# Optimization experiments

Measured on AMD Instinct MI355X. Metric: run time of the kernel, lower is better.

## Reference

```python
import jax, jax.numpy as jnp
import numpy as np

SEQ_LEN, BATCH, INPUT, HID, LAYERS, TARGET_LEN = 120, 2048, 6, 64, 4, 120


def _cell(x_t, h, c, Wih, Whh, b):
    # torch LSTM gate order: input, forget, cell(g), output
    gates = x_t @ Wih.T + h @ Whh.T + b  # [B, 4H]
    i, f, g, o = jnp.split(gates, 4, axis=-1)
    c_new = jax.nn.sigmoid(f) * c + jax.nn.sigmoid(i) * jnp.tanh(g)
    h_new = jax.nn.sigmoid(o) * jnp.tanh(c_new)
    return h_new, c_new


def _stack_step(h, c, x_t, Wih0, Wih, Whh, b):
    # one time step through all stacked layers; h, c: [L, B, H]
    hs, cs = [], []
    inp = x_t
    L = Whh.shape[0]
    for l in range(L):
        W = Wih0 if l == 0 else Wih[l - 1]
        hn, cn = _cell(inp, h[l], c[l], W, Whh[l], b[l])
        hs.append(hn)
        cs.append(cn)
        inp = hn
    return jnp.stack(hs), jnp.stack(cs), inp


def setup_inputs() -> dict:
    key = jax.random.key(0)
    ks = jax.random.split(key, 11)
    s = 1.0 / np.sqrt(HID)  # torch LSTM uniform init scale
    u = lambda k, shp: jax.random.uniform(k, shp, jnp.float32, -s, s)
    return {
        "x": jax.random.normal(ks[0], (SEQ_LEN, BATCH, INPUT), jnp.float32),
        "enc_Wih0": u(ks[1], (4 * HID, INPUT)),
        "enc_Wih": u(ks[2], (LAYERS - 1, 4 * HID, HID)),
        "enc_Whh": u(ks[3], (LAYERS, 4 * HID, HID)),
        "enc_b": u(ks[4], (LAYERS, 4 * HID)),
        "dec_Wih0": u(ks[5], (4 * HID, INPUT)),
        "dec_Wih": u(ks[6], (LAYERS - 1, 4 * HID, HID)),
        "dec_Whh": u(ks[7], (LAYERS, 4 * HID, HID)),
        "dec_b": u(ks[8], (LAYERS, 4 * HID)),
        "lin_W": u(ks[9], (INPUT, HID)),
        "lin_b": u(ks[10], (INPUT,)),
        "target_len": TARGET_LEN,
    }


def reference(x, enc_Wih0, enc_Wih, enc_Whh, enc_b,
              dec_Wih0, dec_Wih, dec_Whh, dec_b, lin_W, lin_b, target_len):
    L, B, H = enc_Whh.shape[0], x.shape[1], enc_Whh.shape[-1]
    h0 = jnp.zeros((L, B, H), x.dtype)

    # ---- encoder: stacked LSTM over the input sequence (zero init state) ----
    def enc_step(carry, x_t):
        h, c = carry
        h, c, _ = _stack_step(h, c, x_t, enc_Wih0, enc_Wih, enc_Whh, enc_b)
        return (h, c), None

    (h, c), _ = jax.lax.scan(enc_step, (h0, h0), x)

    # ---- decoder: recursive one-step decode for target_len steps ----
    def dec_step(carry, _):
        h, c, inp = carry
        h, c, top = _stack_step(h, c, inp, dec_Wih0, dec_Wih, dec_Whh, dec_b)
        out = top @ lin_W.T + lin_b  # [B, INPUT]
        return (h, c, out), out

    last_in = x[-1]  # decoder seeded with last observed frame
    _, outputs = jax.lax.scan(dec_step, (h, c, last_in), None, length=target_len)
    return outputs  # [target_len, B, INPUT]
```

## Files before the change

### kernel.cpp

```cpp
#include <hip/hip_runtime.h>


#define S_LEN 120
#define BATCH 2048
#define NIN   6
#define H     64
#define NL    4
#define TLEN  120

#define HPAD 72

#define FRAGS_HALF 60
#define PACK_H8    (2 * FRAGS_HALF * 4 * 64)
#define PROJ_H8    (2 * 64)
#define NPACK      ((PACK_H8 + PROJ_H8) * 8)
#define EPACK_EL   (256 * 64 * 8)
#define NTOT       (NPACK + EPACK_EL)

#define PERM(kk) ((((kk) & 3) << 4) | ((kk) >> 2))
#define PI(c)    ((((c) & 15) << 2) | ((c) >> 4))

typedef _Float16 h8    __attribute__((ext_vector_type(8)));
typedef _Float16 h4    __attribute__((ext_vector_type(4)));
typedef float    f32x4 __attribute__((ext_vector_type(4)));

__device__ __forceinline__ void bar_lgkm() {
  asm volatile("s_waitcnt lgkmcnt(0)\n\ts_barrier" ::: "memory");
}

__global__ void prep_weights(const float* __restrict__ eWih0,
                             const float* __restrict__ eWih,
                             const float* __restrict__ eWhh,
                             const float* __restrict__ dWih0,
                             const float* __restrict__ dWih,
                             const float* __restrict__ dWhh,
                             const float* __restrict__ linW,
                             _Float16* __restrict__ wq) {
  int idx = blockIdx.x * blockDim.x + threadIdx.x;
  if (idx >= NTOT) return;

  if (idx >= NPACK) {
    int p    = idx - NPACK;
    int j    = p & 7;
    int lane = (p >> 3) & 63;
    int fe   = p >> 9;
    int kt   = fe & 3, nt = (fe >> 2) & 15, l = fe >> 6;
    int g    = nt * 16 + (lane & 15);
    int koff = ((lane >> 4) << 3) + j;
    float v = 0.0f;
    if (l == 0) {
      if (kt == 0)      v = (koff < NIN) ? eWih0[g * NIN + koff] : 0.0f;
      else if (kt == 1) v = 0.0f;
      else { int kk = (kt - 2) * 32 + koff; v = eWhh[g * H + PERM(kk)]; }
    } else {
      if (kt < 2) { int kk = kt * 32 + koff;
                    v = eWih[((l - 1) * 256 + g) * H + PERM(kk)]; }
      else        { int kk = (kt - 2) * 32 + koff;
                    v = eWhh[(l * 256 + g) * H + PERM(kk)]; }
    }
    wq[idx] = (_Float16)v;
    return;
  }

  if (idx >= PACK_H8 * 8) {
    int p    = idx - PACK_H8 * 8;
    int j    = p & 7;
    int lane = (p >> 3) & 63;
    int fr   = p >> 9;
    int m    = lane & 15;
    int k    = fr * 32 + ((lane >> 4) << 3) + j;
    wq[idx] = (_Float16)((m < NIN) ? linW[m * H + k] : 0.0f);
    return;
  }

  const int j    = idx & 7;
  const int lane = (idx >> 3) & 63;
  const int wv   = (idx >> 9) & 3;
  const int fh   = idx >> 11;
  const int f    = fh % FRAGS_HALF;
  const int half = fh / FRAGS_HALF;
  const float* Wi0 = half ? dWih0 : eWih0;
  const float* Wi  = half ? dWih  : eWih;
  const float* Wh  = half ? dWhh  : eWhh;
  int l, q, kt;
  if (f < 12) { l = 0; q = f / 3; kt = f % 3; }
  else        { int ff = f - 12; l = 1 + ff / 16; ff %= 16; q = ff / 4; kt = ff % 4; }
  const int g    = q * 64 + wv * 16 + (lane & 15);
  const int k_in = ((lane >> 4) << 3) + j;
  float v;
  if (l == 0) {
    if (kt == 0) v = (k_in < NIN) ? Wi0[g * NIN + k_in] : 0.0f;
    else         v = Wh[g * H + (kt - 1) * 32 + k_in];
  } else {
    if (kt < 2) v = Wi[((l - 1) * 256 + g) * H + kt * 32 + k_in];
    else        v = Wh[(l * 256 + g) * H + (kt - 2) * 32 + k_in];
  }
  wq[idx] = (_Float16)v;
}

__device__ __forceinline__ float rcpf(float x) { return __builtin_amdgcn_rcpf(x); }
__device__ __forceinline__ f32x4 mf(h8 a, h8 b, f32x4 c) {
  return __builtin_amdgcn_mfma_f32_16x16x32_f16(a, b, c, 0, 0, 0);
}
#define SPLAT(v) ((f32x4){(v), (v), (v), (v)})

__device__ __forceinline__ float ew_one(float gi, float gf, float gg, float go,
                                        float& c) {
  gg = fminf(fmaxf(gg, -20.0f), 20.0f);
  float eni = __expf(-gi);
  float e2g = __expf(2.0f * gg);
  float enf = __expf(-gf);
  float eno = __expf(-go);
  c = c * rcpf(1.0f + enf) + (e2g - 1.0f) * rcpf((1.0f + eni) * (e2g + 1.0f));
  float cc = fminf(fmaxf(c, -20.0f), 20.0f);
  float e2c = __expf(2.0f * cc);
  return (e2c - 1.0f) * rcpf((1.0f + eno) * (e2c + 1.0f));
}

__device__ __forceinline__ void cell_ew(f32x4 g0, f32x4 g1, f32x4 g2, f32x4 g3,
                                        f32x4& c, _Float16* outbuf,
                                        int quad, int r16, int wv) {
  #pragma unroll
  for (int r = 0; r < 4; r++) {
    float cv = c[r];
    float hv = ew_one(g0[r], g1[r], g2[r], g3[r], cv);
    c[r] = cv;
    outbuf[(quad * 4 + r) * HPAD + wv * 16 + r16] = (_Float16)hv;
  }
}
__device__ __forceinline__ void fireH(const h8 (&w)[16], h8 ai0, h8 ai1,
                                      const f32x4 (&ac)[4], f32x4& c,
                                      _Float16* outbuf, int quad, int r16, int wv) {
  f32x4 g0 = mf(ai1, w[1],  mf(ai0, w[0],  ac[0]));
  f32x4 g1 = mf(ai1, w[5],  mf(ai0, w[4],  ac[1]));
  f32x4 g2 = mf(ai1, w[9],  mf(ai0, w[8],  ac[2]));
  f32x4 g3 = mf(ai1, w[13], mf(ai0, w[12], ac[3]));
  cell_ew(g0, g1, g2, g3, c, outbuf, quad, r16, wv);
}
__device__ __forceinline__ void precH(const h8 (&w)[16], h8 ar0, h8 ar1,
                                      f32x4 b, f32x4 (&ac)[4]) {
  ac[0] = mf(ar1, w[3],  mf(ar0, w[2],  SPLAT(b[0])));
  ac[1] = mf(ar1, w[7],  mf(ar0, w[6],  SPLAT(b[1])));
  ac[2] = mf(ar1, w[11], mf(ar0, w[10], SPLAT(b[2])));
  ac[3] = mf(ar1, w[15], mf(ar0, w[14], SPLAT(b[3])));
}
__device__ __forceinline__ void fire0(const h8 (&w)[12], h8 ax,
                                      const f32x4 (&ac)[4], f32x4& c,
                                      _Float16* outbuf, int quad, int r16, int wv) {
  f32x4 g0 = mf(ax, w[0], ac[0]);
  f32x4 g1 = mf(ax, w[3], ac[1]);
  f32x4 g2 = mf(ax, w[6], ac[2]);
  f32x4 g3 = mf(ax, w[9], ac[3]);
  cell_ew(g0, g1, g2, g3, c, outbuf, quad, r16, wv);
}
__device__ __forceinline__ void prec0(const h8 (&w)[12], h8 ar0, h8 ar1,
                                      f32x4 b, f32x4 (&ac)[4]) {
  ac[0] = mf(ar1, w[2],  mf(ar0, w[1],  SPLAT(b[0])));
  ac[1] = mf(ar1, w[5],  mf(ar0, w[4],  SPLAT(b[1])));
  ac[2] = mf(ar1, w[8],  mf(ar0, w[7],  SPLAT(b[2])));
  ac[3] = mf(ar1, w[11], mf(ar0, w[10], SPLAT(b[3])));
}
__device__ __forceinline__ void readA(const _Float16* buf, int r16, int quad,
                                      h8& a0, h8& a1) {
  a0 = *(const h8*)(buf + r16 * HPAD + quad * 8);
  a1 = *(const h8*)(buf + r16 * HPAD + 32 + quad * 8);
}

__global__ void __launch_bounds__(256, 1)
lstm_main(const float* __restrict__ X,
          const float* __restrict__ encb,
          const float* __restrict__ decb,
          const float* __restrict__ linb,
          const h8* __restrict__ WQ,
          float* __restrict__ out) {
  __shared__ _Float16 Hb[NL][2][16][HPAD];
  __shared__ _Float16 Xb[2][16][HPAD];
  __shared__ float    Cx[NL][16][68];

  const int tid   = threadIdx.x;
  const int wv    = tid >> 6;
  const int lane  = tid & 63;
  const int quad  = lane >> 4;
  const int r16   = lane & 15;
  const int bbase = blockIdx.x * 16;

  {
    float* p = (float*)&Hb[0][0][0][0];
    for (int i = tid; i < (int)(NL * 2 * 16 * HPAD / 2); i += 256) p[i] = 0.0f;
    float* px = (float*)&Xb[0][0][0];
    for (int i = tid; i < (int)(2 * 16 * HPAD / 2); i += 256) px[i] = 0.0f;
  }
  if (tid < 96) {
    const int m = tid / NIN, i = tid - m * NIN;
    Xb[0][m][i] = (_Float16)X[((size_t)0 * BATCH + bbase + m) * NIN + i];
  }

  h8 we[16][4];
  #pragma unroll
  for (int nt = 0; nt < 16; nt++)
    #pragma unroll
    for (int kt = 0; kt < 4; kt++)
      we[nt][kt] = WQ[(PACK_H8 + PROJ_H8) + ((wv * 64 + nt * 4 + kt) * 64 + lane)];

  float ben[16];
  #pragma unroll
  for (int nt = 0; nt < 16; nt++) ben[nt] = encb[wv * 256 + nt * 16 + r16];

  f32x4 ce[4];
  #pragma unroll
  for (int ct = 0; ct < 4; ct++) ce[ct] = SPLAT(0.f);

  const bool pfLane = (wv == 0) && (lane < 48);
  const int pe0 = lane * 2, pe1 = pe0 + 1;
  const int pm0 = pe0 / NIN, pc0 = pe0 % NIN;
  const int pm1 = pe1 / NIN, pc1 = pe1 % NIN;
  float pf0 = 0.f, pf1 = 0.f;
  if (pfLane) {
    const float* xs = X + ((size_t)1 * BATCH + bbase) * NIN;
    pf0 = xs[pe0]; pf1 = xs[pe1];
  }

  __syncthreads();

  #pragma unroll 1
  for (int i = 0; i < S_LEN + NL - 1; i++) {
    const int p = i & 1;
    const bool active = (i >= wv) && (i - wv < S_LEN);
    if (active) {
      const _Float16* inb = (wv == 0) ? &Xb[p][0][0] : &Hb[wv - 1][p ^ 1][0][0];
      const _Float16* rcb = &Hb[wv][p ^ 1][0][0];
      h8 ai0 = *(const h8*)(inb + r16 * HPAD + quad * 8);
      h8 ai1 = *(const h8*)(inb + r16 * HPAD + 32 + quad * 8);
      h8 ar0 = *(const h8*)(rcb + r16 * HPAD + quad * 8);
      h8 ar1 = *(const h8*)(rcb + r16 * HPAD + 32 + quad * 8);

      float nf0 = 0.f, nf1 = 0.f;
      if (pfLane && (i + 2 < S_LEN)) {
        const float* xs = X + ((size_t)(i + 2) * BATCH + bbase) * NIN;
        nf0 = xs[pe0]; nf1 = xs[pe1];
      }

      f32x4 acc[16];
      #pragma unroll
      for (int nt = 0; nt < 16; nt++) {
        f32x4 a = SPLAT(ben[nt]);
        a = mf(ai0, we[nt][0], a);
        a = mf(ai1, we[nt][1], a);
        a = mf(ar0, we[nt][2], a);
        a = mf(ar1, we[nt][3], a);
        acc[nt] = a;
      }

      _Float16* wb = &Hb[wv][p][0][0];
      #pragma unroll
      for (int r = 0; r < 4; r++) {
        h4 hv;
        #pragma unroll
        for (int ct = 0; ct < 4; ct++) {
          float cv = ce[ct][r];
          hv[ct] = (_Float16)ew_one(acc[ct][r], acc[4 + ct][r],
                                    acc[8 + ct][r], acc[12 + ct][r], cv);
          ce[ct][r] = cv;
        }
        *(h4*)(wb + (quad * 4 + r) * HPAD + 4 * r16) = hv;
      }

      if (pfLane && (i + 1 < S_LEN)) {
        Xb[p ^ 1][pm0][pc0] = (_Float16)pf0;
        Xb[p ^ 1][pm1][pc1] = (_Float16)pf1;
      }
      pf0 = nf0; pf1 = nf1;
    }
    bar_lgkm();
  }

  #pragma unroll
  for (int ct = 0; ct < 4; ct++)
    #pragma unroll
    for (int r = 0; r < 4; r++)
      Cx[wv][quad * 4 + r][ct * 16 + r16] = ce[ct][r];

  float hreg[16];
  #pragma unroll
  for (int u = 0; u < 16; u++) {
    int i2 = tid + u * 256;
    int l = i2 >> 10, m = (i2 >> 6) & 15, c = i2 & 63;
    hreg[u] = (float)Hb[l][(l + 1) & 1][m][PI(c)];
  }
  __syncthreads();
  #pragma unroll
  for (int u = 0; u < 16; u++) {
    int i2 = tid + u * 256;
    int l = i2 >> 10, m = (i2 >> 6) & 15, c = i2 & 63;
    Hb[l][1][m][c] = (_Float16)hreg[u];
  }
  __syncthreads();

  f32x4 cs0, cs1, cs2, cs3;
  #pragma unroll
  for (int r = 0; r < 4; r++) {
    cs0[r] = Cx[0][quad * 4 + r][wv * 16 + r16];
    cs1[r] = Cx[1][quad * 4 + r][wv * 16 + r16];
    cs2[r] = Cx[2][quad * 4 + r][wv * 16 + r16];
    cs3[r] = Cx[3][quad * 4 + r][wv * 16 + r16];
  }

  h8 w0[12], w1[16], w2[16], w3[16];
  #pragma unroll
  for (int f = 0; f < 12; f++) w0[f] = WQ[((FRAGS_HALF + f)      * 4 + wv) * 64 + lane];
  #pragma unroll
  for (int f = 0; f < 16; f++) w1[f] = WQ[((FRAGS_HALF + 12 + f) * 4 + wv) * 64 + lane];
  #pragma unroll
  for (int f = 0; f < 16; f++) w2[f] = WQ[((FRAGS_HALF + 28 + f) * 4 + wv) * 64 + lane];
  #pragma unroll
  for (int f = 0; f < 16; f++) w3[f] = WQ[((FRAGS_HALF + 44 + f) * 4 + wv) * 64 + lane];

  f32x4 b0, b1, b2, b3;
  #pragma unroll
  for (int q = 0; q < 4; q++) {
    b0[q] = decb[0 * 256 + q * 64 + wv * 16 + r16];
    b1[q] = decb[1 * 256 + q * 64 + wv * 16 + r16];
    b2[q] = decb[2 * 256 + q * 64 + wv * 16 + r16];
    b3[q] = decb[3 * 256 + q * 64 + wv * 16 + r16];
  }

  h8 lwA0 = WQ[PACK_H8 + lane];
  h8 lwA1 = WQ[PACK_H8 + 64 + lane];
  f32x4 lbq;
  #pragma unroll
  for (int r = 0; r < 4; r++)
    lbq[r] = (quad * 4 + r < NIN) ? linb[quad * 4 + r] : 0.0f;

  f32x4 ac0[4], ac1[4], ac2[4], ac3[4];
  {
    h8 s0, s1;
    readA(&Hb[0][1][0][0], r16, quad, s0, s1); prec0(w0, s0, s1, b0, ac0);
    readA(&Hb[1][1][0][0], r16, quad, s0, s1); precH(w1, s0, s1, b1, ac1);
    readA(&Hb[2][1][0][0], r16, quad, s0, s1); precH(w2, s0, s1, b2, ac2);
  }
  __syncthreads();

  #pragma unroll 1
  for (int t = 0; t < TLEN; t++) {
    const int cur = t & 1, prv = cur ^ 1;
    {
      h8 ar0, ar1;
      readA(&Hb[3][prv][0][0], r16, quad, ar0, ar1);
      h8 ax;
      if (t == 0) {
        ax = *(const h8*)(&Xb[1][0][0] + r16 * HPAD + quad * 8);
      } else {
        f32x4 ap = lbq;
        ap = mf(lwA0, ar0, ap);
        ap = mf(lwA1, ar1, ap);
        if (wv == 0) {
          #pragma unroll
          for (int r = 0; r < 4; r++) {
            const int fm = quad * 4 + r;
            if (fm < NIN)
              out[((size_t)(t - 1) * BATCH + bbase + r16) * NIN + fm] = ap[r];
          }
        }
        float x0 = __shfl(ap[0], r16);
        float x1 = __shfl(ap[1], r16);
        float x2 = __shfl(ap[2], r16);
        float x3 = __shfl(ap[3], r16);
        float x4 = __shfl(ap[0], 16 + r16);
        float x5 = __shfl(ap[1], 16 + r16);
        h8 xa = {};
        xa[0] = (_Float16)x0; xa[1] = (_Float16)x1; xa[2] = (_Float16)x2;
        xa[3] = (_Float16)x3; xa[4] = (_Float16)x4; xa[5] = (_Float16)x5;
        h8 zz = {};
        ax = (quad == 0) ? xa : zz;
      }
      precH(w3, ar0, ar1, b3, ac3);
      fire0(w0, ax, ac0, cs0, &Hb[0][cur][0][0], quad, r16, wv);
      bar_lgkm();
    }
    {
      h8 ai0, ai1;
      readA(&Hb[0][cur][0][0], r16, quad, ai0, ai1);
      fireH(w1, ai0, ai1, ac1, cs1, &Hb[1][cur][0][0], quad, r16, wv);
      prec0(w0, ai0, ai1, b0, ac0);
      bar_lgkm();
    }
    {
      h8 ai0, ai1;
      readA(&Hb[1][cur][0][0], r16, quad, ai0, ai1);
      fireH(w2, ai0, ai1, ac2, cs2, &Hb[2][cur][0][0], quad, r16, wv);
      precH(w1, ai0, ai1, b1, ac1);
      bar_lgkm();
    }
    {
      h8 ai0, ai1;
      readA(&Hb[2][cur][0][0], r16, quad, ai0, ai1);
      fireH(w3, ai0, ai1, ac3, cs3, &Hb[3][cur][0][0], quad, r16, wv);
      precH(w2, ai0, ai1, b2, ac2);
      bar_lgkm();
    }
  }

  if (wv == 0) {
    h8 ar0, ar1;
    readA(&Hb[3][1][0][0], r16, quad, ar0, ar1);
    f32x4 ap = lbq;
    ap = mf(lwA0, ar0, ap);
    ap = mf(lwA1, ar1, ap);
    #pragma unroll
    for (int r = 0; r < 4; r++) {
      const int fm = quad * 4 + r;
      if (fm < NIN)
        out[((size_t)(TLEN - 1) * BATCH + bbase + r16) * NIN + fm] = ap[r];
    }
  }
}

extern "C" void kernel_launch(void* const* d_in, const int* in_sizes, int n_in,
                              void* d_out, int out_size, void* d_ws, size_t ws_size,
                              hipStream_t stream) {
  const float* X     = (const float*)d_in[0];
  const float* eWih0 = (const float*)d_in[1];
  const float* eWih  = (const float*)d_in[2];
  const float* eWhh  = (const float*)d_in[3];
  const float* eb    = (const float*)d_in[4];
  const float* dWih0 = (const float*)d_in[5];
  const float* dWih  = (const float*)d_in[6];
  const float* dWhh  = (const float*)d_in[7];
  const float* db    = (const float*)d_in[8];
  const float* lW    = (const float*)d_in[9];
  const float* lb    = (const float*)d_in[10];

  _Float16* wq = (_Float16*)d_ws;

  prep_weights<<<(NTOT + 255) / 256, 256, 0, stream>>>(
      eWih0, eWih, eWhh, dWih0, dWih, dWhh, lW, wq);

  lstm_main<<<BATCH / 16, 256, 0, stream>>>(
      X, eb, db, lb, (const h8*)wq, (float*)d_out);
}
```

Before: 593.4 us.

## Process 32 batch rows per block with 8 waves splitting encoder gate columns

Blocks now cover 32 batch rows with 512 threads instead of 16 rows with 256. In the encoder, two wave groups each take half of every layer's gate columns and loop over two 16-row batch tiles. This halves the per-wave register weight footprint so two blocks can share a CU, and layer 0 skips the zero-padded input MFMA. The decoder keeps its per-group layout. The reorganisation adds shuffling of cell state through shared memory and more synchronisation, and launches half as many blocks, which may reduce parallelism across the GPU.

```diff
diff --git a/kernel.cpp b/kernel.cpp
--- a/kernel.cpp
+++ b/kernel.cpp
@@ -7,6 +7,7 @@
 #define H     64
 #define NL    4
 #define TLEN  120
+#define BB    32
 
 #define HPAD 72
 
@@ -21,7 +22,7 @@
 #define PI(c)    ((((c) & 15) << 2) | ((c) >> 4))
 
 typedef _Float16 h8    __attribute__((ext_vector_type(8)));
-typedef _Float16 h4    __attribute__((ext_vector_type(4)));
+typedef _Float16 hh2   __attribute__((ext_vector_type(2)));
 typedef float    f32x4 __attribute__((ext_vector_type(4)));
 
 __device__ __forceinline__ void bar_lgkm() {
@@ -119,23 +120,23 @@
 
 __device__ __forceinline__ void cell_ew(f32x4 g0, f32x4 g1, f32x4 g2, f32x4 g3,
                                         f32x4& c, _Float16* outbuf,
-                                        int quad, int r16, int wv) {
+                                        int quad, int r16, int lw) {
   #pragma unroll
   for (int r = 0; r < 4; r++) {
     float cv = c[r];
     float hv = ew_one(g0[r], g1[r], g2[r], g3[r], cv);
     c[r] = cv;
-    outbuf[(quad * 4 + r) * HPAD + wv * 16 + r16] = (_Float16)hv;
+    outbuf[(quad * 4 + r) * HPAD + lw * 16 + r16] = (_Float16)hv;
   }
 }
 __device__ __forceinline__ void fireH(const h8 (&w)[16], h8 ai0, h8 ai1,
                                       const f32x4 (&ac)[4], f32x4& c,
-                                      _Float16* outbuf, int quad, int r16, int wv) {
+                                      _Float16* outbuf, int quad, int r16, int lw) {
   f32x4 g0 = mf(ai1, w[1],  mf(ai0, w[0],  ac[0]));
   f32x4 g1 = mf(ai1, w[5],  mf(ai0, w[4],  ac[1]));
   f32x4 g2 = mf(ai1, w[9],  mf(ai0, w[8],  ac[2]));
   f32x4 g3 = mf(ai1, w[13], mf(ai0, w[12], ac[3]));
-  cell_ew(g0, g1, g2, g3, c, outbuf, quad, r16, wv);
+  cell_ew(g0, g1, g2, g3, c, outbuf, quad, r16, lw);
 }
 __device__ __forceinline__ void precH(const h8 (&w)[16], h8 ar0, h8 ar1,
                                       f32x4 b, f32x4 (&ac)[4]) {
@@ -146,12 +147,12 @@
 }
 __device__ __forceinline__ void fire0(const h8 (&w)[12], h8 ax,
                                       const f32x4 (&ac)[4], f32x4& c,
-                                      _Float16* outbuf, int quad, int r16, int wv) {
+                                      _Float16* outbuf, int quad, int r16, int lw) {
   f32x4 g0 = mf(ax, w[0], ac[0]);
   f32x4 g1 = mf(ax, w[3], ac[1]);
   f32x4 g2 = mf(ax, w[6], ac[2]);
   f32x4 g3 = mf(ax, w[9], ac[3]);
-  cell_ew(g0, g1, g2, g3, c, outbuf, quad, r16, wv);
+  cell_ew(g0, g1, g2, g3, c, outbuf, quad, r16, lw);
 }
 __device__ __forceinline__ void prec0(const h8 (&w)[12], h8 ar0, h8 ar1,
                                       f32x4 b, f32x4 (&ac)[4]) {
@@ -166,57 +167,65 @@
   a1 = *(const h8*)(buf + r16 * HPAD + 32 + quad * 8);
 }
 
-__global__ void __launch_bounds__(256, 1)
+__global__ void __launch_bounds__(512, 2)
 lstm_main(const float* __restrict__ X,
           const float* __restrict__ encb,
           const float* __restrict__ decb,
           const float* __restrict__ linb,
           const h8* __restrict__ WQ,
           float* __restrict__ out) {
-  __shared__ _Float16 Hb[NL][2][16][HPAD];
-  __shared__ _Float16 Xb[2][16][HPAD];
-  __shared__ float    Cx[NL][16][68];
-
-  const int tid   = threadIdx.x;
-  const int wv    = tid >> 6;
-  const int lane  = tid & 63;
-  const int quad  = lane >> 4;
-  const int r16   = lane & 15;
-  const int bbase = blockIdx.x * 16;
+  __shared__ _Float16 Hb[2][NL][2][16][HPAD];
+  __shared__ _Float16 Xb[2][2][16][HPAD];
+
+  const int tid  = threadIdx.x;
+  const int wv   = tid >> 6;
+  const int lane = tid & 63;
+  const int quad = lane >> 4;
+  const int r16  = lane & 15;
+  const int grp  = wv >> 2;
+  const int lw   = wv & 3;
 
   {
-    float* p = (float*)&Hb[0][0][0][0];
-    for (int i = tid; i < (int)(NL * 2 * 16 * HPAD / 2); i += 256) p[i] = 0.0f;
-    float* px = (float*)&Xb[0][0][0];
-    for (int i = tid; i < (int)(2 * 16 * HPAD / 2); i += 256) px[i] = 0.0f;
-  }
-  if (tid < 96) {
-    const int m = tid / NIN, i = tid - m * NIN;
-    Xb[0][m][i] = (_Float16)X[((size_t)0 * BATCH + bbase + m) * NIN + i];
-  }
-
-  h8 we[16][4];
-  #pragma unroll
-  for (int nt = 0; nt < 16; nt++)
+    float* p = (float*)&Hb[0][0][0][0][0];
+    for (int i = tid; i < 9216; i += 512) p[i] = 0.0f;
+    float* px = (float*)&Xb[0][0][0][0];
+    for (int i = tid; i < 2304; i += 512) px[i] = 0.0f;
+  }
+  if (tid < BB * NIN) {
+    int m = tid / NIN, ii = tid - m * NIN;
+    Xb[m >> 4][0][m & 15][ii] =
+        (_Float16)X[((size_t)0 * BATCH + blockIdx.x * BB + m) * NIN + ii];
+  }
+
+  h8 we[8][4];
+  #pragma unroll
+  for (int q = 0; q < 4; q++)
     #pragma unroll
-    for (int kt = 0; kt < 4; kt++)
-      we[nt][kt] = WQ[(PACK_H8 + PROJ_H8) + ((wv * 64 + nt * 4 + kt) * 64 + lane)];
-
-  float ben[16];
-  #pragma unroll
-  for (int nt = 0; nt < 16; nt++) ben[nt] = encb[wv * 256 + nt * 16 + r16];
-
-  f32x4 ce[4];
-  #pragma unroll
-  for (int ct = 0; ct < 4; ct++) ce[ct] = SPLAT(0.f);
-
-  const bool pfLane = (wv == 0) && (lane < 48);
-  const int pe0 = lane * 2, pe1 = pe0 + 1;
-  const int pm0 = pe0 / NIN, pc0 = pe0 % NIN;
-  const int pm1 = pe1 / NIN, pc1 = pe1 % NIN;
+    for (int cc = 0; cc < 2; cc++)
+      #pragma unroll
+      for (int kt = 0; kt < 4; kt++)
+        we[q * 2 + cc][kt] =
+            WQ[(PACK_H8 + PROJ_H8) +
+               ((lw * 64 + (q * 4 + 2 * grp + cc) * 4 + kt) * 64 + lane)];
+  float ben[8];
+  #pragma unroll
+  for (int q = 0; q < 4; q++)
+    #pragma unroll
+    for (int cc = 0; cc < 2; cc++)
+      ben[q * 2 + cc] = encb[lw * 256 + q * 64 + (2 * grp + cc) * 16 + r16];
+
+  f32x4 ce[2][2];
+  ce[0][0] = SPLAT(0.f); ce[0][1] = SPLAT(0.f);
+  ce[1][0] = SPLAT(0.f); ce[1][1] = SPLAT(0.f);
+
+  const int  bbE = blockIdx.x * BB + grp * 16;
+  const bool pfLane = (lw == 0) && (lane < 48);
+  const int  pe0 = lane * 2, pe1 = pe0 + 1;
+  const int  pm0 = pe0 / NIN, pc0 = pe0 % NIN;
+  const int  pm1 = pe1 / NIN, pc1 = pe1 % NIN;
   float pf0 = 0.f, pf1 = 0.f;
   if (pfLane) {
-    const float* xs = X + ((size_t)1 * BATCH + bbase) * NIN;
+    const float* xs = X + ((size_t)1 * BATCH + bbE) * NIN;
     pf0 = xs[pe0]; pf1 = xs[pe1];
   }
 
@@ -225,103 +234,115 @@
   #pragma unroll 1
   for (int i = 0; i < S_LEN + NL - 1; i++) {
     const int p = i & 1;
-    const bool active = (i >= wv) && (i - wv < S_LEN);
+    const bool active = (i >= lw) && (i - lw < S_LEN);
     if (active) {
-      const _Float16* inb = (wv == 0) ? &Xb[p][0][0] : &Hb[wv - 1][p ^ 1][0][0];
-      const _Float16* rcb = &Hb[wv][p ^ 1][0][0];
-      h8 ai0 = *(const h8*)(inb + r16 * HPAD + quad * 8);
-      h8 ai1 = *(const h8*)(inb + r16 * HPAD + 32 + quad * 8);
-      h8 ar0 = *(const h8*)(rcb + r16 * HPAD + quad * 8);
-      h8 ar1 = *(const h8*)(rcb + r16 * HPAD + 32 + quad * 8);
-
       float nf0 = 0.f, nf1 = 0.f;
       if (pfLane && (i + 2 < S_LEN)) {
-        const float* xs = X + ((size_t)(i + 2) * BATCH + bbase) * NIN;
+        const float* xs = X + ((size_t)(i + 2) * BATCH + bbE) * NIN;
         nf0 = xs[pe0]; nf1 = xs[pe1];
       }
-
-      f32x4 acc[16];
       #pragma unroll
-      for (int nt = 0; nt < 16; nt++) {
-        f32x4 a = SPLAT(ben[nt]);
-        a = mf(ai0, we[nt][0], a);
-        a = mf(ai1, we[nt][1], a);
-        a = mf(ar0, we[nt][2], a);
-        a = mf(ar1, we[nt][3], a);
-        acc[nt] = a;
+      for (int mt = 0; mt < 2; mt++) {
+        const _Float16* inb =
+            (lw == 0) ? &Xb[mt][p][0][0] : &Hb[mt][lw - 1][p ^ 1][0][0];
+        const _Float16* rcb = &Hb[mt][lw][p ^ 1][0][0];
+        h8 ai0 = *(const h8*)(inb + r16 * HPAD + quad * 8);
+        h8 ai1 = {};
+        if (lw) ai1 = *(const h8*)(inb + r16 * HPAD + 32 + quad * 8);
+        h8 ar0 = *(const h8*)(rcb + r16 * HPAD + quad * 8);
+        h8 ar1 = *(const h8*)(rcb + r16 * HPAD + 32 + quad * 8);
+        f32x4 a[8];
+        #pragma unroll
+        for (int j = 0; j < 8; j++) {
+          f32x4 t = SPLAT(ben[j]);
+          t = mf(ai0, we[j][0], t);
+          if (lw) t = mf(ai1, we[j][1], t);
+          t = mf(ar0, we[j][2], t);
+          t = mf(ar1, we[j][3], t);
+          a[j] = t;
+        }
+        _Float16* wb = &Hb[mt][lw][p][0][0];
+        #pragma unroll
+        for (int r = 0; r < 4; r++) {
+          hh2 hv;
+          #pragma unroll
+          for (int cc = 0; cc < 2; cc++) {
+            float cv = ce[mt][cc][r];
+            hv[cc] = (_Float16)ew_one(a[cc][r], a[2 + cc][r],
+                                      a[4 + cc][r], a[6 + cc][r], cv);
+            ce[mt][cc][r] = cv;
+          }
+          *(hh2*)(wb + (quad * 4 + r) * HPAD + 4 * r16 + 2 * grp) = hv;
+        }
       }
-
-      _Float16* wb = &Hb[wv][p][0][0];
-      #pragma unroll
-      for (int r = 0; r < 4; r++) {
-        h4 hv;
-        #pragma unroll
-        for (int ct = 0; ct < 4; ct++) {
-          float cv = ce[ct][r];
-          hv[ct] = (_Float16)ew_one(acc[ct][r], acc[4 + ct][r],
-                                    acc[8 + ct][r], acc[12 + ct][r], cv);
-          ce[ct][r] = cv;
-        }
-        *(h4*)(wb + (quad * 4 + r) * HPAD + 4 * r16) = hv;
-      }
-
       if (pfLane && (i + 1 < S_LEN)) {
-        Xb[p ^ 1][pm0][pc0] = (_Float16)pf0;
-        Xb[p ^ 1][pm1][pc1] = (_Float16)pf1;
+        Xb[grp][p ^ 1][pm0][pc0] = (_Float16)pf0;
+        Xb[grp][p ^ 1][pm1][pc1] = (_Float16)pf1;
       }
       pf0 = nf0; pf1 = nf1;
     }
     bar_lgkm();
   }
 
-  #pragma unroll
-  for (int ct = 0; ct < 4; ct++)
+  float hreg[16];
+  #pragma unroll
+  for (int u = 0; u < 16; u++) {
+    int i2 = tid + u * 512;
+    int c = i2 & 63, m = (i2 >> 6) & 15, l = (i2 >> 10) & 3, g = (i2 >> 12) & 1;
+    hreg[u] = (float)Hb[g][l][(l + 1) & 1][m][PI(c)];
+  }
+  __syncthreads();
+  {
+    float* cx = (float*)&Hb[0][0][0][0][0];
     #pragma unroll
-    for (int r = 0; r < 4; r++)
-      Cx[wv][quad * 4 + r][ct * 16 + r16] = ce[ct][r];
-
-  float hreg[16];
+    for (int mt = 0; mt < 2; mt++)
+      #pragma unroll
+      for (int cc = 0; cc < 2; cc++)
+        #pragma unroll
+        for (int r = 0; r < 4; r++)
+          cx[((mt * 4 + lw) * 16 + quad * 4 + r) * 64 +
+             (2 * grp + cc) * 16 + r16] = ce[mt][cc][r];
+  }
+  __syncthreads();
+  f32x4 cs0, cs1, cs2, cs3;
+  {
+    const float* cx = (const float*)&Hb[0][0][0][0][0];
+    #pragma unroll
+    for (int r = 0; r < 4; r++) {
+      cs0[r] = cx[((grp * 4 + 0) * 16 + quad * 4 + r) * 64 + lw * 16 + r16];
+      cs1[r] = cx[((grp * 4 + 1) * 16 + quad * 4 + r) * 64 + lw * 16 + r16];
+      cs2[r] = cx[((grp * 4 + 2) * 16 + quad * 4 + r) * 64 + lw * 16 + r16];
+      cs3[r] = cx[((grp * 4 + 3) * 16 + quad * 4 + r) * 64 + lw * 16 + r16];
+    }
+  }
+  __syncthreads();
   #pragma unroll
   for (int u = 0; u < 16; u++) {
-    int i2 = tid + u * 256;
-    int l = i2 >> 10, m = (i2 >> 6) & 15, c = i2 & 63;
-    hreg[u] = (float)Hb[l][(l + 1) & 1][m][PI(c)];
-  }
-  __syncthreads();
-  #pragma unroll
-  for (int u = 0; u < 16; u++) {
-    int i2 = tid + u * 256;
-    int l = i2 >> 10, m = (i2 >> 6) & 15, c = i2 & 63;
-    Hb[l][1][m][c] = (_Float16)hreg[u];
-  }
-  __syncthreads();
-
-  f32x4 cs0, cs1, cs2, cs3;
-  #pragma unroll
-  for (int r = 0; r < 4; r++) {
-    cs0[r] = Cx[0][quad * 4 + r][wv * 16 + r16];
-    cs1[r] = Cx[1][quad * 4 + r][wv * 16 + r16];
-    cs2[r] = Cx[2][quad * 4 + r][wv * 16 + r16];
-    cs3[r] = Cx[3][quad * 4 + r][wv * 16 + r16];
-  }
+    int i2 = tid + u * 512;
+    int c = i2 & 63, m = (i2 >> 6) & 15, l = (i2 >> 10) & 3, g = (i2 >> 12) & 1;
+    Hb[g][l][1][m][c] = (_Float16)hreg[u];
+  }
+  __syncthreads();
+
+  const int bbase = blockIdx.x * BB + grp * 16;
 
   h8 w0[12], w1[16], w2[16], w3[16];
   #pragma unroll
-  for (int f = 0; f < 12; f++) w0[f] = WQ[((FRAGS_HALF + f)      * 4 + wv) * 64 + lane];
-  #pragma unroll
-  for (int f = 0; f < 16; f++) w1[f] = WQ[((FRAGS_HALF + 12 + f) * 4 + wv) * 64 + lane];
-  #pragma unroll
-  for (int f = 0; f < 16; f++) w2[f] = WQ[((FRAGS_HALF + 28 + f) * 4 + wv) * 64 + lane];
-  #pragma unroll
-  for (int f = 0; f < 16; f++) w3[f] = WQ[((FRAGS_HALF + 44 + f) * 4 + wv) * 64 + lane];
+  for (int f = 0; f < 12; f++) w0[f] = WQ[((FRAGS_HALF + f)      * 4 + lw) * 64 + lane];
+  #pragma unroll
+  for (int f = 0; f < 16; f++) w1[f] = WQ[((FRAGS_HALF + 12 + f) * 4 + lw) * 64 + lane];
+  #pragma unroll
+  for (int f = 0; f < 16; f++) w2[f] = WQ[((FRAGS_HALF + 28 + f) * 4 + lw) * 64 + lane];
+  #pragma unroll
+  for (int f = 0; f < 16; f++) w3[f] = WQ[((FRAGS_HALF + 44 + f) * 4 + lw) * 64 + lane];
 
   f32x4 b0, b1, b2, b3;
   #pragma unroll
   for (int q = 0; q < 4; q++) {
-    b0[q] = decb[0 * 256 + q * 64 + wv * 16 + r16];
-    b1[q] = decb[1 * 256 + q * 64 + wv * 16 + r16];
-    b2[q] = decb[2 * 256 + q * 64 + wv * 16 + r16];
-    b3[q] = decb[3 * 256 + q * 64 + wv * 16 + r16];
+    b0[q] = decb[0 * 256 + q * 64 + lw * 16 + r16];
+    b1[q] = decb[1 * 256 + q * 64 + lw * 16 + r16];
+    b2[q] = decb[2 * 256 + q * 64 + lw * 16 + r16];
+    b3[q] = decb[3 * 256 + q * 64 + lw * 16 + r16];
   }
 
   h8 lwA0 = WQ[PACK_H8 + lane];
@@ -334,9 +355,9 @@
   f32x4 ac0[4], ac1[4], ac2[4], ac3[4];
   {
     h8 s0, s1;
-    readA(&Hb[0][1][0][0], r16, quad, s0, s1); prec0(w0, s0, s1, b0, ac0);
-    readA(&Hb[1][1][0][0], r16, quad, s0, s1); precH(w1, s0, s1, b1, ac1);
-    readA(&Hb[2][1][0][0], r16, quad, s0, s1); precH(w2, s0, s1, b2, ac2);
+    readA(&Hb[grp][0][1][0][0], r16, quad, s0, s1); prec0(w0, s0, s1, b0, ac0);
+    readA(&Hb[grp][1][1][0][0], r16, quad, s0, s1); precH(w1, s0, s1, b1, ac1);
+    readA(&Hb[grp][2][1][0][0], r16, quad, s0, s1); precH(w2, s0, s1, b2, ac2);
   }
   __syncthreads();
 
@@ -345,15 +366,15 @@
     const int cur = t & 1, prv = cur ^ 1;
     {
       h8 ar0, ar1;
-      readA(&Hb[3][prv][0][0], r16, quad, ar0, ar1);
+      readA(&Hb[grp][3][prv][0][0], r16, quad, ar0, ar1);
       h8 ax;
       if (t == 0) {
-        ax = *(const h8*)(&Xb[1][0][0] + r16 * HPAD + quad * 8);
+        ax = *(const h8*)(&Xb[grp][1][0][0] + r16 * HPAD + quad * 8);
       } else {
         f32x4 ap = lbq;
         ap = mf(lwA0, ar0, ap);
         ap = mf(lwA1, ar1, ap);
-        if (wv == 0) {
+        if (lw == 0) {
           #pragma unroll
           for (int r = 0; r < 4; r++) {
             const int fm = quad * 4 + r;
@@ -374,35 +395,35 @@
         ax = (quad == 0) ? xa : zz;
       }
       precH(w3, ar0, ar1, b3, ac3);
-      fire0(w0, ax, ac0, cs0, &Hb[0][cur][0][0], quad, r16, wv);
+      fire0(w0, ax, ac0, cs0, &Hb[grp][0][cur][0][0], quad, r16, lw);
       bar_lgkm();
     }
     {
       h8 ai0, ai1;
-      readA(&Hb[0][cur][0][0], r16, quad, ai0, ai1);
-      fireH(w1, ai0, ai1, ac1, cs1, &Hb[1][cur][0][0], quad, r16, wv);
+      readA(&Hb[grp][0][cur][0][0], r16, quad, ai0, ai1);
+      fireH(w1, ai0, ai1, ac1, cs1, &Hb[grp][1][cur][0][0], quad, r16, lw);
       prec0(w0, ai0, ai1, b0, ac0);
       bar_lgkm();
     }
     {
       h8 ai0, ai1;
-      readA(&Hb[1][cur][0][0], r16, quad, ai0, ai1);
-      fireH(w2, ai0, ai1, ac2, cs2, &Hb[2][cur][0][0], quad, r16, wv);
+      readA(&Hb[grp][1][cur][0][0], r16, quad, ai0, ai1);
+      fireH(w2, ai0, ai1, ac2, cs2, &Hb[grp][2][cur][0][0], quad, r16, lw);
       precH(w1, ai0, ai1, b1, ac1);
       bar_lgkm();
     }
     {
       h8 ai0, ai1;
-      readA(&Hb[2][cur][0][0], r16, quad, ai0, ai1);
-      fireH(w3, ai0, ai1, ac3, cs3, &Hb[3][cur][0][0], quad, r16, wv);
+      readA(&Hb[grp][2][cur][0][0], r16, quad, ai0, ai1);
+      fireH(w3, ai0, ai1, ac3, cs3, &Hb[grp][3][cur][0][0], quad, r16, lw);
       precH(w2, ai0, ai1, b2, ac2);
       bar_lgkm();
     }
   }
 
-  if (wv == 0) {
+  if (lw == 0) {
     h8 ar0, ar1;
-    readA(&Hb[3][1][0][0], r16, quad, ar0, ar1);
+    readA(&Hb[grp][3][1][0][0], r16, quad, ar0, ar1);
     f32x4 ap = lbq;
     ap = mf(lwA0, ar0, ap);
     ap = mf(lwA1, ar1, ap);
@@ -435,6 +456,6 @@
   prep_weights<<<(NTOT + 255) / 256, 256, 0, stream>>>(
       eWih0, eWih, eWhh, dWih0, dWih, dWhh, lW, wq);
 
-  lstm_main<<<BATCH / 16, 256, 0, stream>>>(
+  lstm_main<<<BATCH / BB, 512, 0, stream>>>(
       X, eb, db, lb, (const h8*)wq, (float*)d_out);
 }
```

Result: slower. 1.869 ms (+215.0%).
